# Performance work log

Hardware: AMD Instinct MI355X
Metric: run time of the kernel (lower is better)

## Reference

```python
import jax, jax.numpy as jnp
import numpy as np

WIN = (2, 2, 8, 8)
NUM_HEADS = 6
DIM = 120
HID = int(DIM * 2.0)
SHAPE = (8, 4, 64, 64, DIM)


def _layernorm(x, w, b, eps=1e-5):
    m = jnp.mean(x, axis=-1, keepdims=True)
    v = jnp.mean((x - m) ** 2, axis=-1, keepdims=True)
    return (x - m) / jnp.sqrt(v + eps) * w + b


def _window_partition(x, win):
    N, D, H, W, C = x.shape
    x = x.reshape(N // win[0], win[0], D // win[1], win[1],
                  H // win[2], win[2], W // win[3], win[3], C)
    x = jnp.transpose(x, (0, 2, 4, 6, 1, 3, 5, 7, 8))
    return x.reshape(-1, win[0] * win[1] * win[2] * win[3], C)


def _window_reverse(wins, win, N, D, H, W):
    x = wins.reshape(N // win[0], D // win[1], H // win[2], W // win[3],
                     win[0], win[1], win[2], win[3], -1)
    x = jnp.transpose(x, (0, 4, 1, 5, 2, 6, 3, 7, 8))
    return x.reshape(N, D, H, W, -1)


def _mha(q, k, v, scale):
    # q,k,v: (B_, h, n, hd) -> (B_, n, h*hd)
    a = jax.nn.softmax(jnp.einsum('bhid,bhjd->bhij', q * scale, k), axis=-1)
    o = jnp.einsum('bhij,bhjd->bhid', a, v)
    B, h, n, hd = o.shape
    return jnp.transpose(o, (0, 2, 1, 3)).reshape(B, n, h * hd)


def _qkv(xw, W, b, heads):
    B, n, C = xw.shape
    qkv = (xw @ W.T + b).reshape(B, n, 3, heads, C // heads)
    qkv = jnp.transpose(qkv, (2, 0, 3, 1, 4))
    return qkv[0], qkv[1], qkv[2]


def _tmsa(x, norm1_w, norm1_b, qkv_self_w, qkv_self_b, qkv_mut_w, qkv_mut_b,
          proj_w, proj_b, norm2_w, norm2_b, fc11_w, fc11_b, fc12_w, fc12_b,
          fc2_w, fc2_b):
    N, D, H, W, C = x.shape
    heads = NUM_HEADS
    scale = (C // heads) ** -0.5
    # --- attention branch (no shift -> no roll, no mask; dims divide window -> no pad) ---
    h = _layernorm(x, norm1_w, norm1_b)
    xw = _window_partition(h, WIN)                       # (B_, n, C)
    q, k, v = _qkv(xw, qkv_self_w, qkv_self_b, heads)
    x_self = _mha(q, k, v, scale)                        # (B_, n, C)
    q, k, v = _qkv(xw, qkv_mut_w, qkv_mut_b, heads)
    n = xw.shape[1]
    q1, q2 = q[:, :, :n // 2], q[:, :, n // 2:]
    k1, k2 = k[:, :, :n // 2], k[:, :, n // 2:]
    v1, v2 = v[:, :, :n // 2], v[:, :, n // 2:]
    x1 = _mha(q2, k1, v1, scale)                         # (B_, n/2, C)
    x2 = _mha(q1, k2, v2, scale)
    x_mut = jnp.concatenate([x1, x2], axis=1)            # (B_, n, C)
    x_out = jnp.concatenate([x_mut, x_self], axis=2)     # (B_, n, 2C)
    attn = x_out @ proj_w.T + proj_b                     # (B_, n, C)
    attn = _window_reverse(attn, WIN, N, D, H, W)
    x = x + attn
    # --- GEGLU MLP branch ---
    h2 = _layernorm(x, norm2_w, norm2_b)
    gate = jax.nn.gelu(h2 @ fc11_w.T + fc11_b, approximate=False)
    hid = gate * (h2 @ fc12_w.T + fc12_b)
    x = x + (hid @ fc2_w.T + fc2_b)
    return x


def setup_inputs() -> dict:
    key = jax.random.key(0)
    ks = jax.random.split(key, 8)
    s = 0.02
    return {
        'x': jax.random.normal(ks[0], SHAPE, dtype=jnp.float32),
        'norm1_w': jnp.ones((DIM,), jnp.float32),
        'norm1_b': jnp.zeros((DIM,), jnp.float32),
        'qkv_self_w': jax.random.normal(ks[1], (3 * DIM, DIM), jnp.float32) * s,
        'qkv_self_b': jnp.zeros((3 * DIM,), jnp.float32),
        'qkv_mut_w': jax.random.normal(ks[2], (3 * DIM, DIM), jnp.float32) * s,
        'qkv_mut_b': jnp.zeros((3 * DIM,), jnp.float32),
        'proj_w': jax.random.normal(ks[3], (DIM, 2 * DIM), jnp.float32) * s,
        'proj_b': jnp.zeros((DIM,), jnp.float32),
        'norm2_w': jnp.ones((DIM,), jnp.float32),
        'norm2_b': jnp.zeros((DIM,), jnp.float32),
        'fc11_w': jax.random.normal(ks[4], (HID, DIM), jnp.float32) * s,
        'fc11_b': jnp.zeros((HID,), jnp.float32),
        'fc12_w': jax.random.normal(ks[5], (HID, DIM), jnp.float32) * s,
        'fc12_b': jnp.zeros((HID,), jnp.float32),
        'fc2_w': jax.random.normal(ks[6], (DIM, HID), jnp.float32) * s,
        'fc2_b': jnp.zeros((DIM,), jnp.float32),
    }


def reference(x, norm1_w, norm1_b, qkv_self_w, qkv_self_b, qkv_mut_w,
              qkv_mut_b, proj_w, proj_b, norm2_w, norm2_b, fc11_w, fc11_b,
              fc12_w, fc12_b, fc2_w, fc2_b):
    return _tmsa(x, norm1_w, norm1_b, qkv_self_w, qkv_self_b, qkv_mut_w,
                 qkv_mut_b, proj_w, proj_b, norm2_w, norm2_b, fc11_w, fc11_b,
                 fc12_w, fc12_b, fc2_w, fc2_b)
```

## Files before the change

### kernel.cpp

```cpp
#include <hip/hip_runtime.h>
#include <hip/hip_bf16.h>
#include <math.h>


typedef __attribute__((ext_vector_type(8))) short bf16x8;
typedef __attribute__((ext_vector_type(4))) float f32x4;

#define SCALE2 (0.22360679774997896f * 1.44269504088896340f)
#define CHROWS 65536
#define QPLANE 7864320u

union B8U { bf16x8 v; uint4 u4; uint2 u2[2]; unsigned u[4]; short s[8]; };

__device__ __forceinline__ short bf16b(float f) {
    __hip_bfloat16 h = __float2bfloat16(f);
    return *reinterpret_cast<short*>(&h);
}
__device__ __forceinline__ float bf2f(short s) {
    return __uint_as_float(((unsigned)(unsigned short)s) << 16);
}
__device__ __forceinline__ unsigned packbf(float a, float b) {
    return (unsigned)(unsigned short)bf16b(a) |
           ((unsigned)(unsigned short)bf16b(b) << 16);
}

__device__ __forceinline__ int swz(int idx) { return idx ^ ((idx >> 4) & 7); }

__device__ __forceinline__ int rev_row(int r) {
    int w = r >> 8, t = r & 255;
    int w8 = w & 7, h8 = (w >> 3) & 7, d2 = (w >> 6) & 1, n2 = w >> 7;
    int www = t & 7, hh = (t >> 3) & 7, dd = (t >> 6) & 1, nn = t >> 7;
    int n = n2 * 2 + nn, d = d2 * 2 + dd;
    int Hc = h8 * 8 + hh, Wc = w8 * 8 + www;
    return ((n * 4 + d) << 12) + (Hc << 6) + Wc;
}
__device__ __forceinline__ int part_row(int g) {
    int ww = g & 63, hh = (g >> 6) & 63, d = (g >> 12) & 3, n = g >> 14;
    int w = ((n >> 1) * 2 + (d >> 1)) * 64 + ((hh >> 3) << 3) + (ww >> 3);
    int t = (((n & 1) * 2 + (d & 1)) << 6) + ((hh & 7) << 3) + (ww & 7);
    return (w << 8) + t;
}
__device__ __forceinline__ float gelu_exact(float x) {
    return 0.5f * x * (1.0f + erff(x * 0.70710678118654752f));
}

__device__ __forceinline__ bf16x8 load_frag20(const short* row, int quad) {
    B8U r;
    const uint2* p = (const uint2*)(row + quad * 8);
    r.u2[0] = p[0]; r.u2[1] = p[1];
    if (quad == 2) { r.u[2] = 0; r.u[3] = 0; }
    else if (quad == 3) { r.u[0] = r.u[1] = r.u[2] = r.u[3] = 0; }
    return r.v;
}

template <int K>
__device__ __forceinline__ void stageW_frag(uint4* Wf, const float* __restrict__ W,
                                            int bn, int N, int tid) {
    constexpr int CH   = (K == 120) ? 16 : 32;
    constexpr int NKT  = CH / 4;
    constexpr int ITER = 64 * CH / 256;
#pragma unroll
    for (int i = 0; i < ITER; ++i) {
        int c = i * 256 + tid;
        int row = c / CH, q = c % CH;
        int wr = bn + row; if (wr > N - 1) wr = N - 1;
        uint4 d = make_uint4(0u, 0u, 0u, 0u);
        if (q * 8 < K) {
            f32x4 w0 = *(const f32x4*)(W + (size_t)wr * K + q * 8);
            f32x4 w1 = *(const f32x4*)(W + (size_t)wr * K + q * 8 + 4);
            d = make_uint4(packbf(w0.x, w0.y), packbf(w0.z, w0.w),
                           packbf(w1.x, w1.y), packbf(w1.z, w1.w));
        }
        Wf[swz(((row >> 4) * NKT + (q >> 2)) * 64 + (q & 3) * 16 + (row & 15))] = d;
    }
}

template <bool REMAP>
__global__ __launch_bounds__(256) void ln_kernel(const float* __restrict__ in,
                                                 const float* __restrict__ w,
                                                 const float* __restrict__ b,
                                                 short* __restrict__ out) {
    int row  = blockIdx.x * 4 + (threadIdx.x >> 6);
    int lane = threadIdx.x & 63;
    const float* xr = in + (size_t)row * 120;
    float2 v = make_float2(0.f, 0.f);
    if (lane < 60) v = *(const float2*)(xr + lane * 2);
    float s = v.x + v.y;
#pragma unroll
    for (int off = 32; off; off >>= 1) s += __shfl_down(s, off, 64);
    s = __shfl(s, 0, 64);
    float mean = s * (1.f / 120.f);
    float dx = v.x - mean, dy = v.y - mean;
    float q = (lane < 60) ? (dx * dx + dy * dy) : 0.f;
#pragma unroll
    for (int off = 32; off; off >>= 1) q += __shfl_down(q, off, 64);
    q = __shfl(q, 0, 64);
    float rstd = rsqrtf(q * (1.f / 120.f) + 1e-5f);
    int orow = REMAP ? part_row(row) : row;
    if (lane < 60) {
        float2 wv = *(const float2*)(w + lane * 2);
        float2 bv = *(const float2*)(b + lane * 2);
        unsigned u = packbf(dx * rstd * wv.x + bv.x, dy * rstd * wv.y + bv.y);
        *(unsigned*)(out + (size_t)orow * 120 + lane * 2) = u;
    }
}

template <int MODE, int K, int N>
__global__ __launch_bounds__(256) void mm(const short* __restrict__ A,
                                          const float* __restrict__ W,
                                          const float* __restrict__ bias,
                                          void* __restrict__ outp,
                                          const float* __restrict__ aux,
                                          int m0) {
    constexpr int NKT = (K + 31) / 32;
    __shared__ uint4 Wf[4 * NKT * 64];
    const int tid = threadIdx.x;
    const int lane = tid & 63, wave = tid >> 6;
    const int quad = lane >> 4, l16 = lane & 15;
    const int bm  = blockIdx.x * 128 + (wave >> 1) * 64;
    const int bnb = blockIdx.y * 64;
    const int wtile = (wave & 1) * 2;

    stageW_frag<K>(Wf, W, bnb, N, tid);

    const short* Ar[4];
#pragma unroll
    for (int i = 0; i < 4; ++i) Ar[i] = A + (size_t)(bm + i * 16 + l16) * K;

    f32x4 acc[4][2];
#pragma unroll
    for (int i = 0; i < 4; ++i)
#pragma unroll
        for (int j = 0; j < 2; ++j) acc[i][j] = (f32x4){0.f, 0.f, 0.f, 0.f};

    __syncthreads();
#pragma unroll
    for (int kt = 0; kt < NKT; ++kt) {
        int k = kt * 32 + quad * 8;
        int kc = (k + 8 <= K) ? k : 0;
        B8U b0, b1;
        b0.u4 = Wf[swz(((wtile + 0) * NKT + kt) * 64 + lane)];
        b1.u4 = Wf[swz(((wtile + 1) * NKT + kt) * 64 + lane)];
#pragma unroll
        for (int i = 0; i < 4; ++i) {
            bf16x8 a = *(const bf16x8*)(Ar[i] + kc);
            acc[i][0] = __builtin_amdgcn_mfma_f32_16x16x32_bf16(a, b0.v, acc[i][0], 0, 0, 0);
            acc[i][1] = __builtin_amdgcn_mfma_f32_16x16x32_bf16(a, b1.v, acc[i][1], 0, 0, 0);
        }
    }

#pragma unroll
    for (int j = 0; j < 2; ++j) {
        const int n = bnb + wtile * 16 + j * 16 + l16;
        if (n >= N) continue;
        const float bs = bias[n];
        int which = 0, head = 0, e = 0;
        if (MODE == 0) { which = n / 120; int hn = n % 120; head = hn / 20; e = hn % 20; }
#pragma unroll
        for (int i = 0; i < 4; ++i) {
#pragma unroll
            for (int r = 0; r < 4; ++r) {
                int m = bm + i * 16 + quad * 4 + r;
                float val = acc[i][j][r] + bs;
                if (MODE == 0) {
                    if (which == 0) val *= SCALE2;
                    int wl = m >> 8, t = m & 255;
                    ((short*)outp)[(size_t)which * QPLANE +
                                   ((size_t)((wl * 6 + head) * 256 + t)) * 20 + e] = bf16b(val);
                } else if (MODE == 1) {
                    int g = rev_row(m0 + m);
                    val += aux[(size_t)g * 120 + n];
                    ((float*)outp)[(size_t)(m0 + m) * 120 + n] = val;
                } else {
                    int g = rev_row(m0 + m);
                    val += aux[(size_t)m * 120 + n];
                    ((float*)outp)[(size_t)g * 120 + n] = val;
                }
            }
        }
    }
}

__global__ __launch_bounds__(256) void mm_mlp(const short* __restrict__ A,
                                              const float* __restrict__ W1,
                                              const float* __restrict__ b1,
                                              const float* __restrict__ W2,
                                              const float* __restrict__ b2,
                                              short* __restrict__ outp) {
    __shared__ uint4 Wf[2][4 * 4 * 64];
    const int tid = threadIdx.x;
    const int lane = tid & 63, wave = tid >> 6;
    const int quad = lane >> 4, l16 = lane & 15;
    const int bm  = blockIdx.x * 128 + (wave >> 1) * 64;
    const int bnb = blockIdx.y * 64;
    const int wtile = (wave & 1) * 2;
    const int N = 240;

    stageW_frag<120>(Wf[0], W1, bnb, N, tid);
    stageW_frag<120>(Wf[1], W2, bnb, N, tid);

    const short* Ar[4];
#pragma unroll
    for (int i = 0; i < 4; ++i) Ar[i] = A + (size_t)(bm + i * 16 + l16) * 120;

    f32x4 acc1[4][2], acc2[4][2];
#pragma unroll
    for (int i = 0; i < 4; ++i)
#pragma unroll
        for (int j = 0; j < 2; ++j) {
            acc1[i][j] = (f32x4){0.f, 0.f, 0.f, 0.f};
            acc2[i][j] = (f32x4){0.f, 0.f, 0.f, 0.f};
        }

    __syncthreads();
#pragma unroll
    for (int kt = 0; kt < 4; ++kt) {
        int k = kt * 32 + quad * 8;
        int kc = (k + 8 <= 120) ? k : 0;
        B8U p0, p1, q0, q1;
        p0.u4 = Wf[0][swz(((wtile + 0) * 4 + kt) * 64 + lane)];
        p1.u4 = Wf[0][swz(((wtile + 1) * 4 + kt) * 64 + lane)];
        q0.u4 = Wf[1][swz(((wtile + 0) * 4 + kt) * 64 + lane)];
        q1.u4 = Wf[1][swz(((wtile + 1) * 4 + kt) * 64 + lane)];
#pragma unroll
        for (int i = 0; i < 4; ++i) {
            bf16x8 a = *(const bf16x8*)(Ar[i] + kc);
            acc1[i][0] = __builtin_amdgcn_mfma_f32_16x16x32_bf16(a, p0.v, acc1[i][0], 0, 0, 0);
            acc1[i][1] = __builtin_amdgcn_mfma_f32_16x16x32_bf16(a, p1.v, acc1[i][1], 0, 0, 0);
            acc2[i][0] = __builtin_amdgcn_mfma_f32_16x16x32_bf16(a, q0.v, acc2[i][0], 0, 0, 0);
            acc2[i][1] = __builtin_amdgcn_mfma_f32_16x16x32_bf16(a, q1.v, acc2[i][1], 0, 0, 0);
        }
    }

#pragma unroll
    for (int j = 0; j < 2; ++j) {
        const int n = bnb + wtile * 16 + j * 16 + l16;
        if (n >= N) continue;
        const float g1 = b1[n], g2 = b2[n];
#pragma unroll
        for (int i = 0; i < 4; ++i) {
#pragma unroll
            for (int r = 0; r < 4; ++r) {
                int m = bm + i * 16 + quad * 4 + r;
                float gv = acc1[i][j][r] + g1;
                float vv = acc2[i][j][r] + g2;
                outp[(size_t)m * 240 + n] = bf16b(gelu_exact(gv) * vv);
            }
        }
    }
}

template <int NK, bool MUT>
__global__ __launch_bounds__(NK) void attn_flash(const short* __restrict__ qkv,
                                                 short* __restrict__ xout) {
    constexpr int NKT = NK / 32;
    constexpr int VSTR2 = NK + 4;
    __shared__ __align__(16) short Kf[NKT * 2 * 48 * 8];
    __shared__ __align__(16) unsigned Vt2[11 * VSTR2];
    const int b = blockIdx.x;
    int wl, hd, half;
    if (MUT) { half = b & 1; hd = (b >> 1) % 6; wl = b / 12; }
    else     { half = 0;     hd = b % 6;        wl = b / 6;  }
    const int tid  = threadIdx.x;
    const int lane = tid & 63, wave = tid >> 6;
    const int quad = lane >> 4, l16 = lane & 15;

    const size_t rb = (size_t)(wl * 6 + hd) * 256;
    const short* qpl = qkv + rb * 20;
    const short* kpl = qkv + (size_t)QPLANE + rb * 20;
    const short* vpl = qkv + 2 * (size_t)QPLANE + rb * 20;
    const int koff = MUT ? half * 128 : 0;
    const int qoff = MUT ? (1 - half) * 128 : 0;

    {
        const uint2* p = (const uint2*)(vpl + (size_t)(koff + tid) * 20);
        unsigned tmp[10];
#pragma unroll
        for (int i = 0; i < 5; ++i) ((uint2*)tmp)[i] = p[i];
#pragma unroll
        for (int i = 0; i < 10; ++i) Vt2[i * VSTR2 + tid] = tmp[i];
        Vt2[10 * VSTR2 + tid] = 0x00003F80u;

        int skt = tid >> 5, sf = (tid >> 4) & 1, sl = tid & 15;
        int srow = koff + skt * 32 + sf * 4 + ((sl >> 2) << 3) + (sl & 3);
        const uint2* kp = (const uint2*)(kpl + (size_t)srow * 20);
        uint2 k0 = kp[0], k1 = kp[1], k2 = kp[2], k3 = kp[3], k4 = kp[4];
        uint4* dst = (uint4*)Kf + ((skt * 2 + sf) * 48 + sl);
        dst[0]  = make_uint4(k0.x, k0.y, k1.x, k1.y);
        dst[16] = make_uint4(k2.x, k2.y, k3.x, k3.y);
        dst[32] = make_uint4(k4.x, k4.y, 0u, 0u);
    }
    __syncthreads();

    const int quadc = quad < 3 ? quad : 2;
    const uint4* kfrag = (const uint4*)Kf + quadc * 16 + l16;
    const unsigned sel = (l16 & 1) ? 0x07060302u : 0x05040100u;
    const unsigned* vbase0 = Vt2 + (l16 >> 1) * VSTR2;
    int r1 = 8 + (l16 >> 1); if (r1 > 10) r1 = 10;
    const unsigned* vbase1 = Vt2 + r1 * VSTR2;
    const f32x4 z4 = {0.f, 0.f, 0.f, 0.f};

#pragma unroll 1
    for (int g = 0; g < 2; ++g) {
        bf16x8 bq0 = load_frag20(qpl + (size_t)(qoff + wave * 64 + (g * 2 + 0) * 16 + l16) * 20, quad);
        bf16x8 bq1 = load_frag20(qpl + (size_t)(qoff + wave * 64 + (g * 2 + 1) * 16 + l16) * 20, quad);

        f32x4 accO[2][2];
        accO[0][0] = z4; accO[0][1] = z4; accO[1][0] = z4; accO[1][1] = z4;

#pragma unroll
        for (int kt = 0; kt < NKT; ++kt) {
            B8U ak0, ak1;
            ak0.u4 = kfrag[(kt * 2 + 0) * 48];
            ak1.u4 = kfrag[(kt * 2 + 1) * 48];
            B8U av0, av1;
            {
                uint4 va = *(const uint4*)(vbase0 + kt * 32 + quad * 8);
                uint4 vb = *(const uint4*)(vbase0 + kt * 32 + quad * 8 + 4);
                av0.u[0] = __builtin_amdgcn_perm(va.y, va.x, sel);
                av0.u[1] = __builtin_amdgcn_perm(va.w, va.z, sel);
                av0.u[2] = __builtin_amdgcn_perm(vb.y, vb.x, sel);
                av0.u[3] = __builtin_amdgcn_perm(vb.w, vb.z, sel);
                uint4 vc = *(const uint4*)(vbase1 + kt * 32 + quad * 8);
                uint4 vd = *(const uint4*)(vbase1 + kt * 32 + quad * 8 + 4);
                av1.u[0] = __builtin_amdgcn_perm(vc.y, vc.x, sel);
                av1.u[1] = __builtin_amdgcn_perm(vc.w, vc.z, sel);
                av1.u[2] = __builtin_amdgcn_perm(vd.y, vd.x, sel);
                av1.u[3] = __builtin_amdgcn_perm(vd.w, vd.z, sel);
            }
#pragma unroll
            for (int t = 0; t < 2; ++t) {
                bf16x8 bqt = t ? bq1 : bq0;
                f32x4 s0 = __builtin_amdgcn_mfma_f32_16x16x32_bf16(ak0.v, bqt, z4, 0, 0, 0);
                f32x4 s1 = __builtin_amdgcn_mfma_f32_16x16x32_bf16(ak1.v, bqt, z4, 0, 0, 0);
                float p0 = __builtin_amdgcn_exp2f(s0[0]), p1 = __builtin_amdgcn_exp2f(s0[1]);
                float p2 = __builtin_amdgcn_exp2f(s0[2]), p3 = __builtin_amdgcn_exp2f(s0[3]);
                float p4 = __builtin_amdgcn_exp2f(s1[0]), p5 = __builtin_amdgcn_exp2f(s1[1]);
                float p6 = __builtin_amdgcn_exp2f(s1[2]), p7 = __builtin_amdgcn_exp2f(s1[3]);
                B8U bp;
                bp.u[0] = packbf(p0, p1);
                bp.u[1] = packbf(p2, p3);
                bp.u[2] = packbf(p4, p5);
                bp.u[3] = packbf(p6, p7);
                accO[t][0] = __builtin_amdgcn_mfma_f32_16x16x32_bf16(av0.v, bp.v, accO[t][0], 0, 0, 0);
                accO[t][1] = __builtin_amdgcn_mfma_f32_16x16x32_bf16(av1.v, bp.v, accO[t][1], 0, 0, 0);
            }
        }

#pragma unroll
        for (int t = 0; t < 2; ++t) {
            int nt = g * 2 + t;
            float l = __shfl(accO[t][1][0], 16 + l16, 64);
            float inv = 1.f / l;
            int tok = (MUT ? half * 128 : 0) + wave * 64 + nt * 16 + l16;
            short* orow = xout + (size_t)(wl * 256 + tok) * 240 + (MUT ? hd * 20 : 120 + hd * 20);
            unsigned lo = packbf(accO[t][0][0] * inv, accO[t][0][1] * inv);
            unsigned hi2 = packbf(accO[t][0][2] * inv, accO[t][0][3] * inv);
            *(uint2*)(orow + quad * 4) = make_uint2(lo, hi2);
            if (quad == 0) {
                unsigned lo2 = packbf(accO[t][1][0] * inv, accO[t][1][1] * inv);
                unsigned hi3 = packbf(accO[t][1][2] * inv, accO[t][1][3] * inv);
                *(uint2*)(orow + 16) = make_uint2(lo2, hi3);
            }
        }
    }
}

extern "C" void kernel_launch(void* const* d_in, const int* in_sizes, int n_in,
                              void* d_out, int out_size, void* d_ws, size_t ws_size,
                              hipStream_t stream) {
    const float* x          = (const float*)d_in[0];
    const float* norm1_w    = (const float*)d_in[1];
    const float* norm1_b    = (const float*)d_in[2];
    const float* qkv_self_w = (const float*)d_in[3];
    const float* qkv_self_b = (const float*)d_in[4];
    const float* qkv_mut_w  = (const float*)d_in[5];
    const float* qkv_mut_b  = (const float*)d_in[6];
    const float* proj_w     = (const float*)d_in[7];
    const float* proj_b     = (const float*)d_in[8];
    const float* norm2_w    = (const float*)d_in[9];
    const float* norm2_b    = (const float*)d_in[10];
    const float* fc11_w     = (const float*)d_in[11];
    const float* fc11_b     = (const float*)d_in[12];
    const float* fc12_w     = (const float*)d_in[13];
    const float* fc12_b     = (const float*)d_in[14];
    const float* fc2_w      = (const float*)d_in[15];
    const float* fc2_b      = (const float*)d_in[16];

    if (ws_size < 110100480u) return;

    char* wsb   = (char*)d_ws;
    short* Hb    = (short*)wsb;
    short* QKVc  = (short*)(wsb + 31457280);
    short* XOUTc = (short*)(wsb + 78643200);
    float* TMP   = (float*)wsb;
    short* H2c   = (short*)(wsb + 62914560);
    short* HIDc  = (short*)(wsb + 78643200);
    float* X2    = (float*)d_out;
    float* out   = (float*)d_out;

    ln_kernel<true><<<32768, 256, 0, stream>>>(x, norm1_w, norm1_b, Hb);

    for (int c = 0; c < 2; ++c) {
        int m0 = c * CHROWS;
        const short* Ac = Hb + (size_t)m0 * 120;
        mm<0, 120, 360><<<dim3(512, 6), 256, 0, stream>>>(Ac, qkv_self_w, qkv_self_b,
                                                          QKVc, nullptr, 0);
        attn_flash<256, false><<<1536, 256, 0, stream>>>(QKVc, XOUTc);
        mm<0, 120, 360><<<dim3(512, 6), 256, 0, stream>>>(Ac, qkv_mut_w, qkv_mut_b,
                                                          QKVc, nullptr, 0);
        attn_flash<128, true><<<3072, 128, 0, stream>>>(QKVc, XOUTc);
        mm<1, 240, 120><<<dim3(512, 2), 256, 0, stream>>>(XOUTc, proj_w, proj_b,
                                                          X2, x, m0);
    }

    hipMemcpyAsync(TMP, d_out, 62914560u, hipMemcpyDeviceToDevice, stream);

    for (int c = 0; c < 2; ++c) {
        int m0 = c * CHROWS;
        ln_kernel<false><<<16384, 256, 0, stream>>>(TMP + (size_t)m0 * 120,
                                                    norm2_w, norm2_b, H2c);
        mm_mlp<<<dim3(512, 4), 256, 0, stream>>>(H2c, fc11_w, fc11_b,
                                                 fc12_w, fc12_b, HIDc);
        mm<4, 240, 120><<<dim3(512, 2), 256, 0, stream>>>(HIDc, fc2_w, fc2_b,
                                                          out, TMP + (size_t)m0 * 120, m0);
    }
}
```

Measured before the change: 612.0 us.

## Fuse MLP into per-chunk loop, widen GEMM M-tiles, vectorize layernorm

The proj GEMM now writes its residual result into a per-chunk workspace buffer instead of d_out. This drops the full 62 MB device-to-device memcpy and lets the norm2+MLP stages run inside the same chunk loop while data is still hot in cache. All GEMMs get an MT template parameter set to 8, so each block covers 256 rows and the grid is halved, raising per-wave MFMA work and register pressure. The layernorm handles two rows per wave with float4 loads and half-wave xor reductions.

```diff
diff --git a/kernel.cpp b/kernel.cpp
--- a/kernel.cpp
+++ b/kernel.cpp
@@ -80,32 +80,33 @@
                                                  const float* __restrict__ w,
                                                  const float* __restrict__ b,
                                                  short* __restrict__ out) {
-    int row  = blockIdx.x * 4 + (threadIdx.x >> 6);
-    int lane = threadIdx.x & 63;
+    const int tid = threadIdx.x;
+    const int lane = tid & 63, wave = tid >> 6;
+    const int half = lane >> 5, hl = lane & 31;
+    const int row = blockIdx.x * 8 + wave * 2 + half;
     const float* xr = in + (size_t)row * 120;
-    float2 v = make_float2(0.f, 0.f);
-    if (lane < 60) v = *(const float2*)(xr + lane * 2);
-    float s = v.x + v.y;
-#pragma unroll
-    for (int off = 32; off; off >>= 1) s += __shfl_down(s, off, 64);
-    s = __shfl(s, 0, 64);
+    f32x4 v = (f32x4){0.f, 0.f, 0.f, 0.f};
+    if (hl < 30) v = *(const f32x4*)(xr + hl * 4);
+    float s = (v.x + v.y) + (v.z + v.w);
+#pragma unroll
+    for (int off = 16; off; off >>= 1) s += __shfl_xor(s, off, 32);
     float mean = s * (1.f / 120.f);
-    float dx = v.x - mean, dy = v.y - mean;
-    float q = (lane < 60) ? (dx * dx + dy * dy) : 0.f;
-#pragma unroll
-    for (int off = 32; off; off >>= 1) q += __shfl_down(q, off, 64);
-    q = __shfl(q, 0, 64);
+    float d0 = v.x - mean, d1 = v.y - mean, d2 = v.z - mean, d3 = v.w - mean;
+    float q = (hl < 30) ? (d0 * d0 + d1 * d1) + (d2 * d2 + d3 * d3) : 0.f;
+#pragma unroll
+    for (int off = 16; off; off >>= 1) q += __shfl_xor(q, off, 32);
     float rstd = rsqrtf(q * (1.f / 120.f) + 1e-5f);
     int orow = REMAP ? part_row(row) : row;
-    if (lane < 60) {
-        float2 wv = *(const float2*)(w + lane * 2);
-        float2 bv = *(const float2*)(b + lane * 2);
-        unsigned u = packbf(dx * rstd * wv.x + bv.x, dy * rstd * wv.y + bv.y);
-        *(unsigned*)(out + (size_t)orow * 120 + lane * 2) = u;
-    }
-}
-
-template <int MODE, int K, int N>
+    if (hl < 30) {
+        f32x4 wv = *(const f32x4*)(w + hl * 4);
+        f32x4 bv = *(const f32x4*)(b + hl * 4);
+        unsigned u0 = packbf(d0 * rstd * wv.x + bv.x, d1 * rstd * wv.y + bv.y);
+        unsigned u1 = packbf(d2 * rstd * wv.z + bv.z, d3 * rstd * wv.w + bv.w);
+        *(uint2*)(out + (size_t)orow * 120 + hl * 4) = make_uint2(u0, u1);
+    }
+}
+
+template <int MODE, int K, int N, int MT>
 __global__ __launch_bounds__(256) void mm(const short* __restrict__ A,
                                           const float* __restrict__ W,
                                           const float* __restrict__ bias,
@@ -117,19 +118,19 @@
     const int tid = threadIdx.x;
     const int lane = tid & 63, wave = tid >> 6;
     const int quad = lane >> 4, l16 = lane & 15;
-    const int bm  = blockIdx.x * 128 + (wave >> 1) * 64;
+    const int bm  = blockIdx.x * (MT * 32) + (wave >> 1) * (MT * 16);
     const int bnb = blockIdx.y * 64;
     const int wtile = (wave & 1) * 2;
 
     stageW_frag<K>(Wf, W, bnb, N, tid);
 
-    const short* Ar[4];
-#pragma unroll
-    for (int i = 0; i < 4; ++i) Ar[i] = A + (size_t)(bm + i * 16 + l16) * K;
-
-    f32x4 acc[4][2];
-#pragma unroll
-    for (int i = 0; i < 4; ++i)
+    const short* Ar[MT];
+#pragma unroll
+    for (int i = 0; i < MT; ++i) Ar[i] = A + (size_t)(bm + i * 16 + l16) * K;
+
+    f32x4 acc[MT][2];
+#pragma unroll
+    for (int i = 0; i < MT; ++i)
 #pragma unroll
         for (int j = 0; j < 2; ++j) acc[i][j] = (f32x4){0.f, 0.f, 0.f, 0.f};
 
@@ -142,7 +143,7 @@
         b0.u4 = Wf[swz(((wtile + 0) * NKT + kt) * 64 + lane)];
         b1.u4 = Wf[swz(((wtile + 1) * NKT + kt) * 64 + lane)];
 #pragma unroll
-        for (int i = 0; i < 4; ++i) {
+        for (int i = 0; i < MT; ++i) {
             bf16x8 a = *(const bf16x8*)(Ar[i] + kc);
             acc[i][0] = __builtin_amdgcn_mfma_f32_16x16x32_bf16(a, b0.v, acc[i][0], 0, 0, 0);
             acc[i][1] = __builtin_amdgcn_mfma_f32_16x16x32_bf16(a, b1.v, acc[i][1], 0, 0, 0);
@@ -157,7 +158,7 @@
         int which = 0, head = 0, e = 0;
         if (MODE == 0) { which = n / 120; int hn = n % 120; head = hn / 20; e = hn % 20; }
 #pragma unroll
-        for (int i = 0; i < 4; ++i) {
+        for (int i = 0; i < MT; ++i) {
 #pragma unroll
             for (int r = 0; r < 4; ++r) {
                 int m = bm + i * 16 + quad * 4 + r;
@@ -170,7 +171,7 @@
                 } else if (MODE == 1) {
                     int g = rev_row(m0 + m);
                     val += aux[(size_t)g * 120 + n];
-                    ((float*)outp)[(size_t)(m0 + m) * 120 + n] = val;
+                    ((float*)outp)[(size_t)m * 120 + n] = val;
                 } else {
                     int g = rev_row(m0 + m);
                     val += aux[(size_t)m * 120 + n];
@@ -187,11 +188,12 @@
                                               const float* __restrict__ W2,
                                               const float* __restrict__ b2,
                                               short* __restrict__ outp) {
+    constexpr int MT = 8;
     __shared__ uint4 Wf[2][4 * 4 * 64];
     const int tid = threadIdx.x;
     const int lane = tid & 63, wave = tid >> 6;
     const int quad = lane >> 4, l16 = lane & 15;
-    const int bm  = blockIdx.x * 128 + (wave >> 1) * 64;
+    const int bm  = blockIdx.x * (MT * 32) + (wave >> 1) * (MT * 16);
     const int bnb = blockIdx.y * 64;
     const int wtile = (wave & 1) * 2;
     const int N = 240;
@@ -199,13 +201,13 @@
     stageW_frag<120>(Wf[0], W1, bnb, N, tid);
     stageW_frag<120>(Wf[1], W2, bnb, N, tid);
 
-    const short* Ar[4];
-#pragma unroll
-    for (int i = 0; i < 4; ++i) Ar[i] = A + (size_t)(bm + i * 16 + l16) * 120;
-
-    f32x4 acc1[4][2], acc2[4][2];
-#pragma unroll
-    for (int i = 0; i < 4; ++i)
+    const short* Ar[MT];
+#pragma unroll
+    for (int i = 0; i < MT; ++i) Ar[i] = A + (size_t)(bm + i * 16 + l16) * 120;
+
+    f32x4 acc1[MT][2], acc2[MT][2];
+#pragma unroll
+    for (int i = 0; i < MT; ++i)
 #pragma unroll
         for (int j = 0; j < 2; ++j) {
             acc1[i][j] = (f32x4){0.f, 0.f, 0.f, 0.f};
@@ -223,7 +225,7 @@
         q0.u4 = Wf[1][swz(((wtile + 0) * 4 + kt) * 64 + lane)];
         q1.u4 = Wf[1][swz(((wtile + 1) * 4 + kt) * 64 + lane)];
 #pragma unroll
-        for (int i = 0; i < 4; ++i) {
+        for (int i = 0; i < MT; ++i) {
             bf16x8 a = *(const bf16x8*)(Ar[i] + kc);
             acc1[i][0] = __builtin_amdgcn_mfma_f32_16x16x32_bf16(a, p0.v, acc1[i][0], 0, 0, 0);
             acc1[i][1] = __builtin_amdgcn_mfma_f32_16x16x32_bf16(a, p1.v, acc1[i][1], 0, 0, 0);
@@ -238,7 +240,7 @@
         if (n >= N) continue;
         const float g1 = b1[n], g2 = b2[n];
 #pragma unroll
-        for (int i = 0; i < 4; ++i) {
+        for (int i = 0; i < MT; ++i) {
 #pragma unroll
             for (int r = 0; r < 4; ++r) {
                 int m = bm + i * 16 + quad * 4 + r;
@@ -393,36 +395,28 @@
     short* Hb    = (short*)wsb;
     short* QKVc  = (short*)(wsb + 31457280);
     short* XOUTc = (short*)(wsb + 78643200);
-    float* TMP   = (float*)wsb;
+    float* TMPc  = (float*)(wsb + 31457280);
     short* H2c   = (short*)(wsb + 62914560);
     short* HIDc  = (short*)(wsb + 78643200);
-    float* X2    = (float*)d_out;
     float* out   = (float*)d_out;
 
-    ln_kernel<true><<<32768, 256, 0, stream>>>(x, norm1_w, norm1_b, Hb);
+    ln_kernel<true><<<16384, 256, 0, stream>>>(x, norm1_w, norm1_b, Hb);
 
     for (int c = 0; c < 2; ++c) {
         int m0 = c * CHROWS;
         const short* Ac = Hb + (size_t)m0 * 120;
-        mm<0, 120, 360><<<dim3(512, 6), 256, 0, stream>>>(Ac, qkv_self_w, qkv_self_b,
-                                                          QKVc, nullptr, 0);
+        mm<0, 120, 360, 8><<<dim3(256, 6), 256, 0, stream>>>(Ac, qkv_self_w, qkv_self_b,
+                                                             QKVc, nullptr, 0);
         attn_flash<256, false><<<1536, 256, 0, stream>>>(QKVc, XOUTc);
-        mm<0, 120, 360><<<dim3(512, 6), 256, 0, stream>>>(Ac, qkv_mut_w, qkv_mut_b,
-                                                          QKVc, nullptr, 0);
+        mm<0, 120, 360, 8><<<dim3(256, 6), 256, 0, stream>>>(Ac, qkv_mut_w, qkv_mut_b,
+                                                             QKVc, nullptr, 0);
         attn_flash<128, true><<<3072, 128, 0, stream>>>(QKVc, XOUTc);
-        mm<1, 240, 120><<<dim3(512, 2), 256, 0, stream>>>(XOUTc, proj_w, proj_b,
-                                                          X2, x, m0);
-    }
-
-    hipMemcpyAsync(TMP, d_out, 62914560u, hipMemcpyDeviceToDevice, stream);
-
-    for (int c = 0; c < 2; ++c) {
-        int m0 = c * CHROWS;
-        ln_kernel<false><<<16384, 256, 0, stream>>>(TMP + (size_t)m0 * 120,
-                                                    norm2_w, norm2_b, H2c);
-        mm_mlp<<<dim3(512, 4), 256, 0, stream>>>(H2c, fc11_w, fc11_b,
+        mm<1, 240, 120, 8><<<dim3(256, 2), 256, 0, stream>>>(XOUTc, proj_w, proj_b,
+                                                             TMPc, x, m0);
+        ln_kernel<false><<<8192, 256, 0, stream>>>(TMPc, norm2_w, norm2_b, H2c);
+        mm_mlp<<<dim3(256, 4), 256, 0, stream>>>(H2c, fc11_w, fc11_b,
                                                  fc12_w, fc12_b, HIDc);
-        mm<4, 240, 120><<<dim3(512, 2), 256, 0, stream>>>(HIDc, fc2_w, fc2_b,
-                                                          out, TMP + (size_t)m0 * 120, m0);
-    }
-}
+        mm<4, 240, 120, 8><<<dim3(256, 2), 256, 0, stream>>>(HIDc, fc2_w, fc2_b,
+                                                             out, TMPc, m0);
+    }
+}
```

Result: faster. 598.7 us (-2.2%).
